# Optimization experiments

Measured on AMD Instinct MI355X. Metric: run time of the kernel, lower is better.

Reference implementation:

```python
import jax, jax.numpy as jnp
import numpy as np

N_ATOMS = 4096
N_ANGLES = 200000


def setup_inputs() -> dict:
    key = jax.random.key(0)
    k1, k2, k3, k4, k5 = jax.random.split(key, 5)
    # pairwise unit direction vectors [N, N, 3]
    vec = jax.random.normal(k1, (N_ATOMS, N_ATOMS, 3), dtype=jnp.float32)
    vec = vec / jnp.linalg.norm(vec, axis=-1, keepdims=True)
    # pairwise distances [N, N], strictly positive
    dist = jax.random.uniform(k2, (N_ATOMS, N_ATOMS), dtype=jnp.float32) * 2.0 + 0.5
    # angle triplets [A, 3]
    coord_idx = jax.random.randint(k3, (N_ANGLES, 3), 0, N_ATOMS)
    # per-angle parameters: k0 (force const) and theta0 (equilibrium angle, rad)
    k0 = jax.random.uniform(k4, (N_ANGLES,), dtype=jnp.float32) * 100.0
    theta0 = jax.random.uniform(k5, (N_ANGLES,), dtype=jnp.float32) * np.float32(np.pi)
    params = jnp.stack([k0, theta0], axis=1)
    forces_out = jnp.zeros((N_ATOMS, 3), dtype=jnp.float32)
    return {
        "dist_mat": dist,
        "vector_mat": vec,
        "forces_out": forces_out,
        "params": params,
        "coord_idx": coord_idx,
        "calc_energy": 1,
        "calc_forces": 1,
    }


def reference(dist_mat, vector_mat, forces_out, params, coord_idx, calc_energy, calc_forces):
    k0 = params[:, 0]
    theta0 = params[:, 1]
    a1 = coord_idx[:, 0]
    a2 = coord_idx[:, 1]
    a3 = coord_idx[:, 2]

    vec21 = vector_mat[a2, a1]            # [A, 3]
    vec23 = vector_mat[a2, a3]            # [A, 3]
    dist21 = dist_mat[a2, a1]             # [A]
    dist23 = dist_mat[a2, a3]             # [A]

    cos_theta = jnp.clip(jnp.sum(vec21 * vec23, axis=1), -1.0, 1.0)
    theta = jnp.arccos(cos_theta)
    delta_theta = theta - theta0

    if calc_energy:
        energy = jnp.sum(k0 * delta_theta * delta_theta)
    else:
        energy = jnp.zeros([1], dtype=forces_out.dtype)

    forces = forces_out
    if calc_forces:
        sin_theta = jnp.sqrt(1.0 - cos_theta * cos_theta)
        # matches torch nan_to_num(nan=0.0): zero out coef where sin_theta == 0
        coef = jnp.where(sin_theta > 0.0,
                         -2.0 * k0 * delta_theta / jnp.maximum(sin_theta, 1e-12),
                         0.0)
        force0 = coef[:, None] * (cos_theta[:, None] * vec21 - vec23) / dist21[:, None]
        force2 = coef[:, None] * (cos_theta[:, None] * vec23 - vec21) / dist23[:, None]
        force1 = -(force0 + force2)
        forces = forces.at[a1].add(force0).at[a2].add(force1).at[a3].add(force2)

    return energy, forces
```

## Files before the change

kernel.cpp:

```cpp
#include <hip/hip_runtime.h>


__global__ void init_out_kernel(float* __restrict__ out,
                                const float* __restrict__ forces0,
                                int nf) {
    int j = blockIdx.x * blockDim.x + threadIdx.x;
    if (j == 0) out[0] = 0.0f;
    if (j < nf) out[1 + j] = forces0[j];
}

__global__ void __launch_bounds__(1024)
angle_kernel(const float* __restrict__ dist,
             const float* __restrict__ vec,
             const float* __restrict__ params,
             const int*   __restrict__ cidx,
             const int*   __restrict__ ce_p,
             const int*   __restrict__ cf_p,
             float* __restrict__ out,
             float* __restrict__ ws,
             int use_ws,
             int n_atoms, int n_angles) {
    extern __shared__ float s_f[];
    __shared__ float s_e;
    const int nf  = n_atoms * 3;
    const int tid = threadIdx.x;

    for (int j = tid; j < nf; j += blockDim.x) s_f[j] = 0.0f;
    if (tid == 0) s_e = 0.0f;
    __syncthreads();

    const int ce = ce_p[0];
    const int cf = cf_p[0];

    float e_acc = 0.0f;
    const long stride = (long)gridDim.x * blockDim.x;
    for (long i = (long)blockIdx.x * blockDim.x + tid; i < n_angles; i += stride) {
        const int a1 = cidx[3 * i + 0];
        const int a2 = cidx[3 * i + 1];
        const int a3 = cidx[3 * i + 2];
        const float k0  = params[2 * i + 0];
        const float th0 = params[2 * i + 1];

        const long b21 = (long)a2 * n_atoms + a1;
        const long b23 = (long)a2 * n_atoms + a3;

        const float v21x = vec[b21 * 3 + 0];
        const float v21y = vec[b21 * 3 + 1];
        const float v21z = vec[b21 * 3 + 2];
        const float v23x = vec[b23 * 3 + 0];
        const float v23y = vec[b23 * 3 + 1];
        const float v23z = vec[b23 * 3 + 2];
        const float d21 = dist[b21];
        const float d23 = dist[b23];

        float c = v21x * v23x + v21y * v23y + v21z * v23z;
        c = fminf(1.0f, fmaxf(-1.0f, c));
        const float th  = acosf(c);
        const float dth = th - th0;

        if (ce) e_acc += k0 * dth * dth;

        if (cf) {
            const float s2 = fmaxf(0.0f, 1.0f - c * c);
            const float s  = sqrtf(s2);
            const float coef = (s > 0.0f) ? (-2.0f * k0 * dth / fmaxf(s, 1e-12f)) : 0.0f;
            const float i21 = coef / d21;
            const float i23 = coef / d23;

            const float f0x = i21 * (c * v21x - v23x);
            const float f0y = i21 * (c * v21y - v23y);
            const float f0z = i21 * (c * v21z - v23z);
            const float f2x = i23 * (c * v23x - v21x);
            const float f2y = i23 * (c * v23y - v21y);
            const float f2z = i23 * (c * v23z - v21z);
            const float f1x = -(f0x + f2x);
            const float f1y = -(f0y + f2y);
            const float f1z = -(f0z + f2z);

            atomicAdd(&s_f[a1 * 3 + 0], f0x);
            atomicAdd(&s_f[a1 * 3 + 1], f0y);
            atomicAdd(&s_f[a1 * 3 + 2], f0z);
            atomicAdd(&s_f[a2 * 3 + 0], f1x);
            atomicAdd(&s_f[a2 * 3 + 1], f1y);
            atomicAdd(&s_f[a2 * 3 + 2], f1z);
            atomicAdd(&s_f[a3 * 3 + 0], f2x);
            atomicAdd(&s_f[a3 * 3 + 1], f2y);
            atomicAdd(&s_f[a3 * 3 + 2], f2z);
        }
    }

    if (ce) {
        for (int off = 32; off > 0; off >>= 1)
            e_acc += __shfl_down(e_acc, off, 64);
        if ((tid & 63) == 0) atomicAdd(&s_e, e_acc);
    }
    __syncthreads();
    if (ce && tid == 0) atomicAdd(&out[0], s_e);

    if (use_ws) {
        float* w = ws + (long)blockIdx.x * nf;
        for (int j = tid; j < nf; j += blockDim.x) w[j] = s_f[j];
    } else if (cf) {
        for (int j = tid; j < nf; j += blockDim.x) {
            const float v = s_f[j];
            if (v != 0.0f) atomicAdd(&out[1 + j], v);
        }
    }
}

#define SEG 16

__global__ void reduce_kernel(const float* __restrict__ ws,
                              float* __restrict__ out,
                              int nf, int n_part) {
    const int comp = blockIdx.x * blockDim.x + threadIdx.x;
    if (comp >= nf) return;
    const int p0 = blockIdx.y * SEG;
    int p1 = p0 + SEG;
    if (p1 > n_part) p1 = n_part;
    float s = 0.0f;
    for (int p = p0; p < p1; ++p)
        s += ws[(long)p * nf + comp];
    if (s != 0.0f) atomicAdd(&out[1 + comp], s);
}

extern "C" void kernel_launch(void* const* d_in, const int* in_sizes, int n_in,
                              void* d_out, int out_size, void* d_ws, size_t ws_size,
                              hipStream_t stream) {
    const float* dist    = (const float*)d_in[0];
    const float* vec     = (const float*)d_in[1];
    const float* forces0 = (const float*)d_in[2];
    const float* params  = (const float*)d_in[3];
    const int*   cidx    = (const int*)d_in[4];
    const int*   ce_p    = (const int*)d_in[5];
    const int*   cf_p    = (const int*)d_in[6];
    float* out = (float*)d_out;

    const int n_atoms  = in_sizes[2] / 3;
    const int n_angles = in_sizes[4] / 3;
    const int nf = n_atoms * 3;

    init_out_kernel<<<(nf + 1 + 255) / 256, 256, 0, stream>>>(out, forces0, nf);

    const size_t partial_bytes = (size_t)nf * sizeof(float);
    int n_part = 256;
    if (ws_size < (size_t)n_part * partial_bytes)
        n_part = (int)(ws_size / partial_bytes);
    const int use_ws = (n_part >= 8) ? 1 : 0;

    const int T = 1024;
    const int B = use_ws ? n_part : 256;
    const size_t lds_bytes = (size_t)nf * sizeof(float);

    angle_kernel<<<B, T, lds_bytes, stream>>>(dist, vec, params, cidx, ce_p, cf_p,
                                              out, (float*)d_ws, use_ws,
                                              n_atoms, n_angles);

    if (use_ws) {
        dim3 grid((nf + 255) / 256, (n_part + SEG - 1) / SEG);
        reduce_kernel<<<grid, 256, 0, stream>>>((const float*)d_ws, out, nf, n_part);
    }
}
```

Baseline: 301.4 us.

## Use one angle per thread and fold init into deterministic partial reduction

The persistent grid-stride loop over 256 blocks is replaced by one thread per angle, launching about 196 blocks of 1024 threads. Per-block energy and force partials go to workspace, and a single reduce kernel adds them to the initial forces. This removes the separate init kernel and the global atomics, and params are loaded as float2. In exchange, every block still zeroes and writes back a full shared-memory force array for only 1024 angles, and the reduce kernel runs each component serially over all partials with small 64-thread blocks.

```diff
diff --git a/kernel.cpp b/kernel.cpp
--- a/kernel.cpp
+++ b/kernel.cpp
@@ -1,31 +1,23 @@
 #include <hip/hip_runtime.h>
 
 
-__global__ void init_out_kernel(float* __restrict__ out,
-                                const float* __restrict__ forces0,
-                                int nf) {
-    int j = blockIdx.x * blockDim.x + threadIdx.x;
-    if (j == 0) out[0] = 0.0f;
-    if (j < nf) out[1 + j] = forces0[j];
-}
-
 __global__ void __launch_bounds__(1024)
-angle_kernel(const float* __restrict__ dist,
-             const float* __restrict__ vec,
-             const float* __restrict__ params,
-             const int*   __restrict__ cidx,
-             const int*   __restrict__ ce_p,
-             const int*   __restrict__ cf_p,
+angle_kernel(const float*  __restrict__ dist,
+             const float*  __restrict__ vec,
+             const float2* __restrict__ params,
+             const int*    __restrict__ cidx,
+             const int*    __restrict__ ce_p,
+             const int*    __restrict__ cf_p,
+             float* __restrict__ ws_f,
+             float* __restrict__ ws_e,
              float* __restrict__ out,
-             float* __restrict__ ws,
-             int use_ws,
              int n_atoms, int n_angles) {
     extern __shared__ float s_f[];
     __shared__ float s_e;
     const int nf  = n_atoms * 3;
     const int tid = threadIdx.x;
 
-    for (int j = tid; j < nf; j += blockDim.x) s_f[j] = 0.0f;
+    for (int j = tid; j < nf; j += 1024) s_f[j] = 0.0f;
     if (tid == 0) s_e = 0.0f;
     __syncthreads();
 
@@ -33,37 +25,35 @@
     const int cf = cf_p[0];
 
     float e_acc = 0.0f;
-    const long stride = (long)gridDim.x * blockDim.x;
-    for (long i = (long)blockIdx.x * blockDim.x + tid; i < n_angles; i += stride) {
+    const int i = blockIdx.x * 1024 + tid;
+    if (i < n_angles) {
         const int a1 = cidx[3 * i + 0];
         const int a2 = cidx[3 * i + 1];
         const int a3 = cidx[3 * i + 2];
-        const float k0  = params[2 * i + 0];
-        const float th0 = params[2 * i + 1];
+        const float2 kt = params[i];
 
-        const long b21 = (long)a2 * n_atoms + a1;
-        const long b23 = (long)a2 * n_atoms + a3;
+        const unsigned row = (unsigned)a2 * (unsigned)n_atoms;
+        const unsigned b21 = row + (unsigned)a1;
+        const unsigned b23 = row + (unsigned)a3;
+        const float* __restrict__ p21 = vec + 3u * b21;
+        const float* __restrict__ p23 = vec + 3u * b23;
 
-        const float v21x = vec[b21 * 3 + 0];
-        const float v21y = vec[b21 * 3 + 1];
-        const float v21z = vec[b21 * 3 + 2];
-        const float v23x = vec[b23 * 3 + 0];
-        const float v23y = vec[b23 * 3 + 1];
-        const float v23z = vec[b23 * 3 + 2];
+        const float v21x = p21[0], v21y = p21[1], v21z = p21[2];
+        const float v23x = p23[0], v23y = p23[1], v23z = p23[2];
         const float d21 = dist[b21];
         const float d23 = dist[b23];
 
         float c = v21x * v23x + v21y * v23y + v21z * v23z;
         c = fminf(1.0f, fmaxf(-1.0f, c));
         const float th  = acosf(c);
-        const float dth = th - th0;
+        const float dth = th - kt.y;
 
-        if (ce) e_acc += k0 * dth * dth;
+        if (ce) e_acc = kt.x * dth * dth;
 
         if (cf) {
             const float s2 = fmaxf(0.0f, 1.0f - c * c);
             const float s  = sqrtf(s2);
-            const float coef = (s > 0.0f) ? (-2.0f * k0 * dth / fmaxf(s, 1e-12f)) : 0.0f;
+            const float coef = (s > 0.0f) ? (-2.0f * kt.x * dth / fmaxf(s, 1e-12f)) : 0.0f;
             const float i21 = coef / d21;
             const float i23 = coef / d23;
 
@@ -89,75 +79,88 @@
         }
     }
 
-    if (ce) {
-        for (int off = 32; off > 0; off >>= 1)
-            e_acc += __shfl_down(e_acc, off, 64);
-        if ((tid & 63) == 0) atomicAdd(&s_e, e_acc);
-    }
+    for (int off = 32; off > 0; off >>= 1)
+        e_acc += __shfl_down(e_acc, off, 64);
+    if ((tid & 63) == 0) atomicAdd(&s_e, e_acc);
     __syncthreads();
-    if (ce && tid == 0) atomicAdd(&out[0], s_e);
 
-    if (use_ws) {
-        float* w = ws + (long)blockIdx.x * nf;
-        for (int j = tid; j < nf; j += blockDim.x) w[j] = s_f[j];
-    } else if (cf) {
-        for (int j = tid; j < nf; j += blockDim.x) {
+    if (ws_f != nullptr) {
+        float* __restrict__ w = ws_f + (size_t)blockIdx.x * nf;
+        for (int j = tid; j < nf; j += 1024) w[j] = s_f[j];
+        if (tid == 0) ws_e[blockIdx.x] = s_e;
+    } else {
+        for (int j = tid; j < nf; j += 1024) {
             const float v = s_f[j];
             if (v != 0.0f) atomicAdd(&out[1 + j], v);
         }
+        if (tid == 0) atomicAdd(&out[0], s_e);
     }
 }
 
-#define SEG 16
+__global__ void __launch_bounds__(64)
+reduce_kernel(const float* __restrict__ ws_f,
+              const float* __restrict__ ws_e,
+              const float* __restrict__ forces0,
+              float* __restrict__ out,
+              int nf, int n_part) {
+    const int j = blockIdx.x * 64 + threadIdx.x;
+    if (j < nf) {
+        float s = forces0[j];
+        for (int p = 0; p < n_part; ++p)
+            s += ws_f[(size_t)p * nf + j];
+        out[1 + j] = s;
+    }
+    if (blockIdx.x == 0) {
+        float e = 0.0f;
+        for (int p = (int)threadIdx.x; p < n_part; p += 64)
+            e += ws_e[p];
+        for (int off = 32; off > 0; off >>= 1)
+            e += __shfl_down(e, off, 64);
+        if (threadIdx.x == 0) out[0] = e;
+    }
+}
 
-__global__ void reduce_kernel(const float* __restrict__ ws,
-                              float* __restrict__ out,
-                              int nf, int n_part) {
-    const int comp = blockIdx.x * blockDim.x + threadIdx.x;
-    if (comp >= nf) return;
-    const int p0 = blockIdx.y * SEG;
-    int p1 = p0 + SEG;
-    if (p1 > n_part) p1 = n_part;
-    float s = 0.0f;
-    for (int p = p0; p < p1; ++p)
-        s += ws[(long)p * nf + comp];
-    if (s != 0.0f) atomicAdd(&out[1 + comp], s);
+__global__ void init_out_kernel(float* __restrict__ out,
+                                const float* __restrict__ forces0,
+                                int nf) {
+    int j = blockIdx.x * blockDim.x + threadIdx.x;
+    if (j == 0) out[0] = 0.0f;
+    if (j < nf) out[1 + j] = forces0[j];
 }
 
 extern "C" void kernel_launch(void* const* d_in, const int* in_sizes, int n_in,
                               void* d_out, int out_size, void* d_ws, size_t ws_size,
                               hipStream_t stream) {
-    const float* dist    = (const float*)d_in[0];
-    const float* vec     = (const float*)d_in[1];
-    const float* forces0 = (const float*)d_in[2];
-    const float* params  = (const float*)d_in[3];
-    const int*   cidx    = (const int*)d_in[4];
-    const int*   ce_p    = (const int*)d_in[5];
-    const int*   cf_p    = (const int*)d_in[6];
+    const float*  dist    = (const float*)d_in[0];
+    const float*  vec     = (const float*)d_in[1];
+    const float*  forces0 = (const float*)d_in[2];
+    const float2* params  = (const float2*)d_in[3];
+    const int*    cidx    = (const int*)d_in[4];
+    const int*    ce_p    = (const int*)d_in[5];
+    const int*    cf_p    = (const int*)d_in[6];
     float* out = (float*)d_out;
 
     const int n_atoms  = in_sizes[2] / 3;
     const int n_angles = in_sizes[4] / 3;
     const int nf = n_atoms * 3;
 
-    init_out_kernel<<<(nf + 1 + 255) / 256, 256, 0, stream>>>(out, forces0, nf);
+    const int n_part = (n_angles + 1023) / 1024;
+    const size_t ws_need = ((size_t)n_part * nf + n_part) * sizeof(float);
+    const bool use_ws = (ws_size >= ws_need);
 
-    const size_t partial_bytes = (size_t)nf * sizeof(float);
-    int n_part = 256;
-    if (ws_size < (size_t)n_part * partial_bytes)
-        n_part = (int)(ws_size / partial_bytes);
-    const int use_ws = (n_part >= 8) ? 1 : 0;
+    float* ws_f = use_ws ? (float*)d_ws : nullptr;
+    float* ws_e = use_ws ? ((float*)d_ws + (size_t)n_part * nf) : nullptr;
 
-    const int T = 1024;
-    const int B = use_ws ? n_part : 256;
     const size_t lds_bytes = (size_t)nf * sizeof(float);
 
-    angle_kernel<<<B, T, lds_bytes, stream>>>(dist, vec, params, cidx, ce_p, cf_p,
-                                              out, (float*)d_ws, use_ws,
-                                              n_atoms, n_angles);
+    if (!use_ws)
+        init_out_kernel<<<(nf + 1 + 255) / 256, 256, 0, stream>>>(out, forces0, nf);
 
-    if (use_ws) {
-        dim3 grid((nf + 255) / 256, (n_part + SEG - 1) / SEG);
-        reduce_kernel<<<grid, 256, 0, stream>>>((const float*)d_ws, out, nf, n_part);
-    }
+    angle_kernel<<<n_part, 1024, lds_bytes, stream>>>(dist, vec, params, cidx,
+                                                      ce_p, cf_p, ws_f, ws_e, out,
+                                                      n_atoms, n_angles);
+
+    if (use_ws)
+        reduce_kernel<<<(nf + 63) / 64, 64, 0, stream>>>(ws_f, ws_e, forces0,
+                                                         out, nf, n_part);
 }
```

After: 338.0 us. 1.12x slower.
